# Optimization experiments

Hardware: AMD Instinct MI355X
Metric: run time of the kernel (lower is better)

The kernel has to match this reference:

```python
import jax, jax.numpy as jnp
import numpy as np

NUM_LEVELS = 16
BASE_RES = 16
T = 1 << 19            # hashmap size per level (log2_hashmap_size=19)
LEVEL_DIM = 2
SCALE = 2.0 ** (np.log2(2048.0 / 16.0) / (NUM_LEVELS - 1))  # desired_resolution=2048
PRIME1 = 2654435761
PRIME2 = 805459861
N_POINTS = 524288


def hash_encode(x, tables):
    # x: [N,3] in [0,1]; tables: [NUM_LEVELS, T, LEVEL_DIM]
    x = jnp.clip(x, 0.0, 1.0)
    feats = []
    for l in range(NUM_LEVELS):
        R = int(np.ceil(BASE_RES * SCALE ** l))
        pos = x * R                      # grid has R+1 vertices per axis
        p0f = jnp.floor(pos)
        w = pos - p0f                    # trilinear weights [N,3]
        p0 = p0f.astype(jnp.uint32)
        dense = (R + 1) ** 3 <= T
        acc = jnp.zeros((x.shape[0], LEVEL_DIM), dtype=tables.dtype)
        for c in range(8):               # 8 cube corners
            off = np.array([(c >> d) & 1 for d in range(3)], dtype=np.uint32)
            idx = jnp.minimum(p0 + off[None, :], jnp.uint32(R))
            if dense:
                flat = idx[:, 0] + jnp.uint32(R + 1) * idx[:, 1] + jnp.uint32((R + 1) ** 2) * idx[:, 2]
            else:
                flat = idx[:, 0] ^ (idx[:, 1] * jnp.uint32(PRIME1)) ^ (idx[:, 2] * jnp.uint32(PRIME2))
                flat = flat & jnp.uint32(T - 1)
            wc = jnp.prod(jnp.where(off[None, :] == 1, w, 1.0 - w), axis=-1)
            acc = acc + wc[:, None] * tables[l, flat]
        feats.append(acc)
    return jnp.concatenate(feats, axis=-1)  # [N, 32]


def pos_embed(x):
    # NeRF embedding: include input + sin/cos of 2^0..2^5 * x -> 3 + 36 = 39 dims
    outs = [x]
    for j in range(6):
        f = float(2 ** j)
        outs.append(jnp.sin(f * x))
        outs.append(jnp.cos(f * x))
    return jnp.concatenate(outs, axis=-1)


def wn_linear(h, v, g, b):
    # weight-norm: W = g * v / ||v||_row
    w = g[:, None] * v / jnp.linalg.norm(v, axis=1, keepdims=True)
    return h @ w.T + b


def softplus100(x):
    return jax.nn.softplus(100.0 * x) / 100.0


def setup_inputs() -> dict:
    key = jax.random.key(0)
    ks = jax.random.split(key, 8)
    x = jax.random.uniform(ks[0], (N_POINTS, 3), dtype=jnp.float32)
    tables = jax.random.uniform(ks[1], (NUM_LEVELS, T, LEVEL_DIM), minval=-1e-4, maxval=1e-4, dtype=jnp.float32)
    d_in_mlp = 3 + 36 + NUM_LEVELS * LEVEL_DIM  # 71
    dims = [d_in_mlp, 256, 256, 257]
    params = {}
    for l in range(3):
        fan_out = dims[l + 1]
        v = jax.random.normal(ks[2 + l], (dims[l + 1], dims[l]), dtype=jnp.float32) * np.sqrt(2.0 / fan_out)
        params[f'v{l}'] = v
        params[f'g{l}'] = jnp.linalg.norm(v, axis=1)  # weight_norm init: g = ||v||
        params[f'b{l}'] = jnp.zeros((dims[l + 1],), dtype=jnp.float32)
    return {'x': x, 'tables': tables, **params}


def reference(x, tables, v0, g0, b0, v1, g1, b1, v2, g2, b2):
    # object_center=0, object_scale=1, divide_factor=1 -> encoder sees x directly
    feat = hash_encode(x, tables)
    inp = jnp.concatenate([pos_embed(x), feat], axis=-1)  # [N, 71]
    h = softplus100(wn_linear(inp, v0, g0, b0))
    h = softplus100(wn_linear(h, v1, g1, b1))
    return wn_linear(h, v2, g2, b2)  # [N, 257] = sdf(1) + feature(256)
```

## Files before the change

### kernel.cpp

```cpp
#include <hip/hip_runtime.h>
#include <math.h>

typedef __bf16 bf16;
typedef __attribute__((ext_vector_type(8))) __bf16 bf16x8;
typedef __attribute__((ext_vector_type(4))) float f32x4;
typedef __attribute__((ext_vector_type(4))) short s16x4;

#define T_HASH (1u << 19)
#define PRIME1 2654435761u
#define PRIME2 805459861u

struct Levels { unsigned R[16]; unsigned mY[16]; unsigned mZ[16]; unsigned df[16]; };

__device__ __forceinline__ unsigned umin_(unsigned a, unsigned b) { return a < b ? a : b; }

__device__ __forceinline__ int swzoff(int row, int colByte) {
    return row * 512 + (colByte ^ ((row & 7) << 4));
}

__device__ __forceinline__ void stb(char* base, int row, int col, float v) {
    *(bf16*)(base + swzoff(row, col * 2)) = (bf16)v;
}
__device__ __forceinline__ void stw(char* base, int row, int col, unsigned short v) {
    *(unsigned short*)(base + swzoff(row, col * 2)) = v;
}

__device__ __forceinline__ float softplus100f(float v) {
    float u = v * 144.2695041f;
    float e = __builtin_amdgcn_exp2f(u);
    float y = __builtin_amdgcn_logf(1.f + e) * 0.006931471806f;
    return v > 0.25f ? v : y;
}

__device__ __forceinline__ unsigned short f2bfu(float v) {
    bf16 h = (bf16)v;
    return *(unsigned short*)&h;
}

__global__ void prep_weights(const float* __restrict__ v0, const float* __restrict__ g0,
                             const float* __restrict__ v1, const float* __restrict__ g1,
                             const float* __restrict__ v2, const float* __restrict__ g2,
                             unsigned short* __restrict__ W0, unsigned short* __restrict__ W1,
                             unsigned short* __restrict__ W2) {
    int r = blockIdx.x;
    int lane = threadIdx.x;
    const float* src = nullptr; const float* g = nullptr; unsigned short* dst; int K, Kp, row;
    if (r < 256)      { row = r;       src = v0 + row * 71;  g = g0; dst = W0 + row * 96;  K = 71;  Kp = 96;  }
    else if (r < 512) { row = r - 256; src = v1 + row * 256; g = g1; dst = W1 + row * 256; K = 256; Kp = 256; }
    else              { row = r - 512; if (row < 257) { src = v2 + row * 256; g = g2; }
                        dst = W2 + row * 256; K = 256; Kp = 256; }
    float ss = 0.f;
    if (src) for (int c = lane; c < K; c += 64) { float v = src[c]; ss += v * v; }
    for (int off = 32; off; off >>= 1) ss += __shfl_down(ss, off);
    ss = __shfl(ss, 0);
    float scale = src ? (g[row] / sqrtf(ss)) : 0.f;
    for (int c = lane; c < Kp; c += 64) {
        float v = (src && c < K) ? src[c] * scale : 0.f;
        dst[c] = f2bfu(v);
    }
}

__global__ void conv_tables(const float2* __restrict__ t, unsigned* __restrict__ tbf) {
    size_t i = (size_t)blockIdx.x * 256 + threadIdx.x;
    float2 e = t[i];
    tbf[i] = (unsigned)f2bfu(e.x) | ((unsigned)f2bfu(e.y) << 16);
}

__global__ __launch_bounds__(256, 8)
void encode_levels(const float* __restrict__ x, const unsigned* __restrict__ tbf,
                   unsigned* __restrict__ featsLM, Levels lv, int npts) {
    const int slot = blockIdx.x & 7, seq = blockIdx.x >> 3;
    const int l = slot + 8 * (seq & 1);
    const int group = seq >> 1;
    const unsigned Ru = lv.R[l], mY = lv.mY[l], mZ = lv.mZ[l];
    const bool dense = lv.df[l] != 0;
    const unsigned* __restrict__ tl = tbf + (size_t)l * T_HASH;
    unsigned* __restrict__ fout = featsLM + (size_t)l * npts;
    const float Rf = (float)Ru;
    const int base = group * 1024 + threadIdx.x;
#pragma unroll
    for (int k = 0; k < 4; ++k) {
        const int p = base + k * 256;
        float xr0 = x[p * 3 + 0], xr1 = x[p * 3 + 1], xr2 = x[p * 3 + 2];
        const float cx = fminf(fmaxf(xr0, 0.f), 1.f);
        const float cy = fminf(fmaxf(xr1, 0.f), 1.f);
        const float cz = fminf(fmaxf(xr2, 0.f), 1.f);
        float px = cx * Rf, py = cy * Rf, pz = cz * Rf;
        float fx = floorf(px), fy = floorf(py), fz = floorf(pz);
        float wx = px - fx, wy = py - fy, wz = pz - fz;
        unsigned ix = (unsigned)fx, iy = (unsigned)fy, iz = (unsigned)fz;
        unsigned xc0 = ix, xc1 = umin_(ix + 1u, Ru);
        unsigned y0 = iy * mY, y1 = umin_(iy + 1u, Ru) * mY;
        unsigned z0 = iz * mZ, z1 = umin_(iz + 1u, Ru) * mZ;
        unsigned yzA[4] = { y0 + z0, y1 + z0, y0 + z1, y1 + z1 };
        float w0x = 1.f - wx, w0y = 1.f - wy, w0z = 1.f - wz;
        float wyz[4] = { w0y * w0z, wy * w0z, w0y * wz, wy * wz };
        float a0 = 0.f, a1 = 0.f;
#pragma unroll
        for (int c = 0; c < 8; ++c) {
            const int ox = c & 1, cyz = c >> 1;
            unsigned xc = ox ? xc1 : xc0;
            unsigned gi = dense ? (xc + yzA[cyz])
                                : ((xc ^ yzA[cyz]) & (T_HASH - 1u));
            unsigned u = tl[gi];
            float ex = __uint_as_float(u << 16);
            float ey = __uint_as_float(u & 0xffff0000u);
            float wc = (ox ? wx : w0x) * wyz[cyz];
            a0 = fmaf(wc, ex, a0);
            a1 = fmaf(wc, ey, a1);
        }
        unsigned outw = (unsigned)f2bfu(a0) | ((unsigned)f2bfu(a1) << 16);
        __builtin_nontemporal_store(outw, &fout[p]);
    }
}


#define STG_STRIDE 260

template<int KSTEPS, int ROWLEN>
__device__ __forceinline__ void layer_mid(const char* __restrict__ inbuf,
                                          const unsigned short* __restrict__ W,
                                          const float* __restrict__ bias,
                                          char* __restrict__ outbuf, int tid) {
    const int lane = tid & 63, wave = tid >> 6;
    const int lrow = lane & 15, lk = lane >> 4;
    const unsigned short* __restrict__ wrow = W + (wave * 16 + lrow) * ROWLEN + lk * 8;
    f32x4 acc[4] = {};
    bf16x8 a_cur = *(const bf16x8*)(wrow);
#pragma unroll
    for (int ks = 0; ks < KSTEPS; ++ks) {
        const int k0 = ks * 32 + lk * 8;
        bf16x8 b[4];
#pragma unroll
        for (int pt = 0; pt < 4; ++pt)
            b[pt] = *(const bf16x8*)(inbuf + swzoff(pt * 16 + lrow, k0 * 2));
        bf16x8 a_next;
        if (ks + 1 < KSTEPS) a_next = *(const bf16x8*)(wrow + (ks + 1) * 32);
#pragma unroll
        for (int pt = 0; pt < 4; ++pt)
            acc[pt] = __builtin_amdgcn_mfma_f32_16x16x32_bf16(a_cur, b[pt], acc[pt], 0, 0, 0);
        a_cur = a_next;
    }
    const int c0 = wave * 16 + lk * 4;
    const float4 bv = *(const float4*)(bias + c0);
#pragma unroll
    for (int pt = 0; pt < 4; ++pt) {
        const int p = pt * 16 + lrow;
        s16x4 o;
        o.x = (short)f2bfu(softplus100f(acc[pt][0] + bv.x));
        o.y = (short)f2bfu(softplus100f(acc[pt][1] + bv.y));
        o.z = (short)f2bfu(softplus100f(acc[pt][2] + bv.z));
        o.w = (short)f2bfu(softplus100f(acc[pt][3] + bv.w));
        *(s16x4*)(outbuf + swzoff(p, c0 * 2)) = o;
    }
}

__device__ __forceinline__ void layer_fin(const char* __restrict__ inbuf,
                                          const unsigned short* __restrict__ W2,
                                          const float* __restrict__ b2,
                                          float* __restrict__ stg,
                                          float* __restrict__ out, int tid, int blk) {
    const int lane = tid & 63, wave = tid >> 6;
    const int lrow = lane & 15, lk = lane >> 4;
    const unsigned short* __restrict__ wrow = W2 + (wave * 16 + lrow) * 256 + lk * 8;
    f32x4 acc[4] = {};
    bf16x8 a_cur = *(const bf16x8*)(wrow);
#pragma unroll
    for (int ks = 0; ks < 8; ++ks) {
        const int k0 = ks * 32 + lk * 8;
        bf16x8 b[4];
#pragma unroll
        for (int pt = 0; pt < 4; ++pt)
            b[pt] = *(const bf16x8*)(inbuf + swzoff(pt * 16 + lrow, k0 * 2));
        bf16x8 a_next;
        if (ks < 7) a_next = *(const bf16x8*)(wrow + (ks + 1) * 32);
#pragma unroll
        for (int pt = 0; pt < 4; ++pt)
            acc[pt] = __builtin_amdgcn_mfma_f32_16x16x32_bf16(a_cur, b[pt], acc[pt], 0, 0, 0);
        a_cur = a_next;
    }
    const int p = tid >> 4, sub = tid & 15;
    float part = 0.f;
    {
        const unsigned short* __restrict__ w2r = W2 + 256 * 256 + sub * 16;
        bf16x8 h0 = *(const bf16x8*)(inbuf + swzoff(p, sub * 32));
        bf16x8 h1 = *(const bf16x8*)(inbuf + swzoff(p, sub * 32 + 16));
        bf16x8 w0 = *(const bf16x8*)(w2r);
        bf16x8 w1 = *(const bf16x8*)(w2r + 8);
#pragma unroll
        for (int j = 0; j < 8; ++j) {
            part = fmaf((float)h0[j], (float)w0[j], part);
            part = fmaf((float)h1[j], (float)w1[j], part);
        }
    }
#pragma unroll
    for (int m = 1; m < 16; m <<= 1) part += __shfl_xor(part, m);

    __syncthreads();
    const int c0 = wave * 16 + lk * 4;
    const float4 bv = *(const float4*)(b2 + c0);
#pragma unroll
    for (int pt = 0; pt < 4; ++pt) {
        const int pr = pt * 16 + lrow;
        f32x4 v;
        v[0] = acc[pt][0] + bv.x;
        v[1] = acc[pt][1] + bv.y;
        v[2] = acc[pt][2] + bv.z;
        v[3] = acc[pt][3] + bv.w;
        *(f32x4*)(stg + pr * STG_STRIDE + c0) = v;
    }
    if (sub == 0) stg[p * STG_STRIDE + 256] = part + b2[256];
    __syncthreads();
    float* __restrict__ dst = out + (size_t)blk * 16448;
#pragma unroll
    for (int r = 0; r < 4; ++r) {
        const int f0 = (r * 1024 + tid) * 4;
        const unsigned pp = ((unsigned)f0 * 65281u) >> 24;
        const int cc = f0 - (int)pp * 257;
        f32x4 v;
#pragma unroll
        for (int u = 0; u < 4; ++u) {
            int c2 = cc + u; unsigned p2 = pp;
            if (c2 >= 257) { c2 -= 257; p2++; }
            v[u] = stg[p2 * STG_STRIDE + c2];
        }
        *(f32x4*)(dst + f0) = v;
    }
    if (tid < 64) {
        const int f0 = 16384 + tid;
        const unsigned pp = ((unsigned)f0 * 65281u) >> 24;
        const int cc = f0 - (int)pp * 257;
        dst[f0] = stg[pp * STG_STRIDE + cc];
    }
}

__global__ __launch_bounds__(1024, 8)
void fused_net(const float* __restrict__ x, const float2* __restrict__ tables,
               const unsigned* __restrict__ featsLM,
               const unsigned short* __restrict__ W0, const unsigned short* __restrict__ W1,
               const unsigned short* __restrict__ W2,
               const float* __restrict__ b0, const float* __restrict__ b1, const float* __restrict__ b2,
               float* __restrict__ out, Levels lv, int npts) {
    __shared__ __align__(16) char smem[66560 + 256];
    unsigned* sR  = (unsigned*)(smem + 66560);
    unsigned* sMY = sR + 16;
    unsigned* sMZ = sR + 32;
    unsigned* sDF = sR + 48;
    char* buf0 = smem;
    char* buf1 = smem + 32768;
    float* stg = (float*)smem;
    const int tid = threadIdx.x;
    const int blk = blockIdx.x;

    if (tid >= 960) {
        int i = tid - 960;
        if (i < 16)      sR[i]  = lv.R[i];
        else if (i < 32) sMY[i - 16] = lv.mY[i - 16];
        else if (i < 48) sMZ[i - 32] = lv.mZ[i - 32];
        else             sDF[i - 48] = lv.df[i - 48];
    }
    __syncthreads();

    const int p = tid >> 4, sub = tid & 15;
    const float xr0 = x[(size_t)blk * 192 + p * 3 + 0];
    const float xr1 = x[(size_t)blk * 192 + p * 3 + 1];
    const float xr2 = x[(size_t)blk * 192 + p * 3 + 2];

    if (sub < 13) {
        int c0 = sub * 3;
#pragma unroll
        for (int u = 0; u < 3; ++u) {
            int c = c0 + u;
            if (c >= 39) break;
            float v;
            if (c < 3) v = (c == 0) ? xr0 : (c == 1 ? xr1 : xr2);
            else {
                int q = c - 3, j = q / 6, k = q - j * 6;
                int axis = (k < 3) ? k : k - 3;
                float xv = axis == 0 ? xr0 : (axis == 1 ? xr1 : xr2);
                float fx = (float)(1 << j) * xv;
                v = (k < 3) ? __sinf(fx) : __cosf(fx);
            }
            stb(buf0, p, c, v);
        }
    }
    for (int c = 71 + sub; c < 96; c += 16) stb(buf0, p, c, 0.f);

    if (featsLM) {
        const int l = sub;
        unsigned u = featsLM[(size_t)l * npts + blk * 64 + p];
        stw(buf0, p, 39 + 2 * l, (unsigned short)(u & 0xffffu));
        stw(buf0, p, 40 + 2 * l, (unsigned short)(u >> 16));
    } else {
        const int l = sub;
        const float cx = fminf(fmaxf(xr0, 0.f), 1.f);
        const float cy = fminf(fmaxf(xr1, 0.f), 1.f);
        const float cz = fminf(fmaxf(xr2, 0.f), 1.f);
        const unsigned Ru = sR[l], mY = sMY[l], mZ = sMZ[l];
        const bool dense = sDF[l] != 0;
        const unsigned lofs = (unsigned)l << 19;
        const float Rf = (float)Ru;
        float px = cx * Rf, py = cy * Rf, pz = cz * Rf;
        float fx = floorf(px), fy = floorf(py), fz = floorf(pz);
        float wx = px - fx, wy = py - fy, wz = pz - fz;
        unsigned ix = (unsigned)fx, iy = (unsigned)fy, iz = (unsigned)fz;
        unsigned xc0 = ix, xc1 = umin_(ix + 1u, Ru);
        unsigned y0 = iy * mY, y1 = umin_(iy + 1u, Ru) * mY;
        unsigned z0 = iz * mZ, z1 = umin_(iz + 1u, Ru) * mZ;
        unsigned yzA[4] = { y0 + z0 + lofs, y1 + z0 + lofs, y0 + z1 + lofs, y1 + z1 + lofs };
        unsigned yzX[4] = { y0 ^ z0, y1 ^ z0, y0 ^ z1, y1 ^ z1 };
        float w0x = 1.f - wx, w0y = 1.f - wy, w0z = 1.f - wz;
        float wyz[4] = { w0y * w0z, wy * w0z, w0y * wz, wy * wz };
        float a0 = 0.f, a1 = 0.f;
#pragma unroll
        for (int c = 0; c < 8; ++c) {
            const int ox = c & 1, cyz = c >> 1;
            unsigned xc = ox ? xc1 : xc0;
            unsigned fd = xc + yzA[cyz];
            unsigned fh = ((xc ^ yzX[cyz]) & (T_HASH - 1u)) + lofs;
            unsigned gi = dense ? fd : fh;
            float2 e2 = tables[gi];
            float wc = (ox ? wx : w0x) * wyz[cyz];
            a0 = fmaf(wc, e2.x, a0);
            a1 = fmaf(wc, e2.y, a1);
        }
        stb(buf0, p, 39 + 2 * l, a0);
        stb(buf0, p, 40 + 2 * l, a1);
    }
    __syncthreads();

    layer_mid<3, 96>(buf0, W0, b0, buf1, tid);
    __syncthreads();
    layer_mid<8, 256>(buf1, W1, b1, buf0, tid);
    __syncthreads();
    layer_fin(buf0, W2, b2, stg, out, tid, blk);
}

extern "C" void kernel_launch(void* const* d_in, const int* in_sizes, int n_in,
                              void* d_out, int out_size, void* d_ws, size_t ws_size,
                              hipStream_t stream) {
    const float*  x      = (const float*)d_in[0];
    const float2* tables = (const float2*)d_in[1];
    const float*  v0 = (const float*)d_in[2];
    const float*  g0 = (const float*)d_in[3];
    const float*  b0 = (const float*)d_in[4];
    const float*  v1 = (const float*)d_in[5];
    const float*  g1 = (const float*)d_in[6];
    const float*  b1 = (const float*)d_in[7];
    const float*  v2 = (const float*)d_in[8];
    const float*  g2 = (const float*)d_in[9];
    const float*  b2 = (const float*)d_in[10];

    unsigned short* W0 = (unsigned short*)d_ws;
    unsigned short* W1 = W0 + 256 * 96;
    unsigned short* W2 = W1 + 256 * 256;
    size_t ofs_tbf   = 319488;
    size_t ofs_feats = ofs_tbf + (size_t)16 * T_HASH * 4;
    size_t need      = ofs_feats + (size_t)16 * T_HASH * 4;
    unsigned* tbf     = (unsigned*)((char*)d_ws + ofs_tbf);
    unsigned* featsLM = (unsigned*)((char*)d_ws + ofs_feats);
    bool use_split = ws_size >= need;

    Levels lv;
    double SCALE = pow(2.0, log2(2048.0 / 16.0) / 15.0);
    for (int l = 0; l < 16; ++l) {
        double r = 16.0 * pow(SCALE, (double)l);
        unsigned R = (unsigned)ceil(r);
        lv.R[l] = R;
        unsigned long long s = (unsigned long long)R + 1;
        int dense = (s * s * s <= (unsigned long long)T_HASH) ? 1 : 0;
        lv.df[l] = dense;
        lv.mY[l] = dense ? (R + 1u) : PRIME1;
        lv.mZ[l] = dense ? (R + 1u) * (R + 1u) : PRIME2;
    }

    prep_weights<<<784, 64, 0, stream>>>(v0, g0, v1, g1, v2, g2, W0, W1, W2);

    int n = in_sizes[0] / 3;
    int nblk = n / 64;

    if (use_split) {
        conv_tables<<<16 * T_HASH / 256, 256, 0, stream>>>(tables, tbf);
        encode_levels<<<8 * (n / 1024) * 2, 256, 0, stream>>>(x, tbf, featsLM, lv, n);
        fused_net<<<nblk, 1024, 0, stream>>>(x, tables, featsLM, W0, W1, W2,
                                             b0, b1, b2, (float*)d_out, lv, n);
    } else {
        fused_net<<<nblk, 1024, 0, stream>>>(x, tables, nullptr, W0, W1, W2,
                                             b0, b1, b2, (float*)d_out, lv, n);
    }
}
```

Baseline: 626.9 us.

## Shrink fused MLP block to 32 points with 2x2 MFMA tiles per wave

```diff
diff --git a/kernel.cpp b/kernel.cpp
--- a/kernel.cpp
+++ b/kernel.cpp
@@ -124,34 +124,44 @@
                                           char* __restrict__ outbuf, int tid) {
     const int lane = tid & 63, wave = tid >> 6;
     const int lrow = lane & 15, lk = lane >> 4;
-    const unsigned short* __restrict__ wrow = W + (wave * 16 + lrow) * ROWLEN + lk * 8;
-    f32x4 acc[4] = {};
-    bf16x8 a_cur = *(const bf16x8*)(wrow);
+    const unsigned short* __restrict__ wr0 = W + (wave * 32 + lrow) * ROWLEN + lk * 8;
+    const unsigned short* __restrict__ wr1 = W + (wave * 32 + 16 + lrow) * ROWLEN + lk * 8;
+    f32x4 acc[2][2] = {};
+    bf16x8 a_cur[2] = { *(const bf16x8*)(wr0), *(const bf16x8*)(wr1) };
 #pragma unroll
     for (int ks = 0; ks < KSTEPS; ++ks) {
         const int k0 = ks * 32 + lk * 8;
-        bf16x8 b[4];
-#pragma unroll
-        for (int pt = 0; pt < 4; ++pt)
+        bf16x8 b[2];
+#pragma unroll
+        for (int pt = 0; pt < 2; ++pt)
             b[pt] = *(const bf16x8*)(inbuf + swzoff(pt * 16 + lrow, k0 * 2));
-        bf16x8 a_next;
-        if (ks + 1 < KSTEPS) a_next = *(const bf16x8*)(wrow + (ks + 1) * 32);
-#pragma unroll
-        for (int pt = 0; pt < 4; ++pt)
-            acc[pt] = __builtin_amdgcn_mfma_f32_16x16x32_bf16(a_cur, b[pt], acc[pt], 0, 0, 0);
-        a_cur = a_next;
-    }
-    const int c0 = wave * 16 + lk * 4;
-    const float4 bv = *(const float4*)(bias + c0);
-#pragma unroll
-    for (int pt = 0; pt < 4; ++pt) {
-        const int p = pt * 16 + lrow;
-        s16x4 o;
-        o.x = (short)f2bfu(softplus100f(acc[pt][0] + bv.x));
-        o.y = (short)f2bfu(softplus100f(acc[pt][1] + bv.y));
-        o.z = (short)f2bfu(softplus100f(acc[pt][2] + bv.z));
-        o.w = (short)f2bfu(softplus100f(acc[pt][3] + bv.w));
-        *(s16x4*)(outbuf + swzoff(p, c0 * 2)) = o;
+        bf16x8 a_next[2];
+        if (ks + 1 < KSTEPS) {
+            a_next[0] = *(const bf16x8*)(wr0 + (ks + 1) * 32);
+            a_next[1] = *(const bf16x8*)(wr1 + (ks + 1) * 32);
+        }
+#pragma unroll
+        for (int mr = 0; mr < 2; ++mr)
+#pragma unroll
+            for (int pt = 0; pt < 2; ++pt)
+                acc[mr][pt] = __builtin_amdgcn_mfma_f32_16x16x32_bf16(a_cur[mr], b[pt], acc[mr][pt], 0, 0, 0);
+        a_cur[0] = a_next[0];
+        a_cur[1] = a_next[1];
+    }
+#pragma unroll
+    for (int mr = 0; mr < 2; ++mr) {
+        const int c0 = wave * 32 + mr * 16 + lk * 4;
+        const float4 bv = *(const float4*)(bias + c0);
+#pragma unroll
+        for (int pt = 0; pt < 2; ++pt) {
+            const int p = pt * 16 + lrow;
+            s16x4 o;
+            o.x = (short)f2bfu(softplus100f(acc[mr][pt][0] + bv.x));
+            o.y = (short)f2bfu(softplus100f(acc[mr][pt][1] + bv.y));
+            o.z = (short)f2bfu(softplus100f(acc[mr][pt][2] + bv.z));
+            o.w = (short)f2bfu(softplus100f(acc[mr][pt][3] + bv.w));
+            *(s16x4*)(outbuf + swzoff(p, c0 * 2)) = o;
+        }
     }
 }
 
@@ -162,22 +172,29 @@
                                           float* __restrict__ out, int tid, int blk) {
     const int lane = tid & 63, wave = tid >> 6;
     const int lrow = lane & 15, lk = lane >> 4;
-    const unsigned short* __restrict__ wrow = W2 + (wave * 16 + lrow) * 256 + lk * 8;
-    f32x4 acc[4] = {};
-    bf16x8 a_cur = *(const bf16x8*)(wrow);
+    const unsigned short* __restrict__ wr0 = W2 + (wave * 32 + lrow) * 256 + lk * 8;
+    const unsigned short* __restrict__ wr1 = W2 + (wave * 32 + 16 + lrow) * 256 + lk * 8;
+    f32x4 acc[2][2] = {};
+    bf16x8 a_cur[2] = { *(const bf16x8*)(wr0), *(const bf16x8*)(wr1) };
 #pragma unroll
     for (int ks = 0; ks < 8; ++ks) {
         const int k0 = ks * 32 + lk * 8;
-        bf16x8 b[4];
-#pragma unroll
-        for (int pt = 0; pt < 4; ++pt)
+        bf16x8 b[2];
+#pragma unroll
+        for (int pt = 0; pt < 2; ++pt)
             b[pt] = *(const bf16x8*)(inbuf + swzoff(pt * 16 + lrow, k0 * 2));
-        bf16x8 a_next;
-        if (ks < 7) a_next = *(const bf16x8*)(wrow + (ks + 1) * 32);
-#pragma unroll
-        for (int pt = 0; pt < 4; ++pt)
-            acc[pt] = __builtin_amdgcn_mfma_f32_16x16x32_bf16(a_cur, b[pt], acc[pt], 0, 0, 0);
-        a_cur = a_next;
+        bf16x8 a_next[2];
+        if (ks < 7) {
+            a_next[0] = *(const bf16x8*)(wr0 + (ks + 1) * 32);
+            a_next[1] = *(const bf16x8*)(wr1 + (ks + 1) * 32);
+        }
+#pragma unroll
+        for (int mr = 0; mr < 2; ++mr)
+#pragma unroll
+            for (int pt = 0; pt < 2; ++pt)
+                acc[mr][pt] = __builtin_amdgcn_mfma_f32_16x16x32_bf16(a_cur[mr], b[pt], acc[mr][pt], 0, 0, 0);
+        a_cur[0] = a_next[0];
+        a_cur[1] = a_next[1];
     }
     const int p = tid >> 4, sub = tid & 15;
     float part = 0.f;
@@ -197,24 +214,27 @@
     for (int m = 1; m < 16; m <<= 1) part += __shfl_xor(part, m);
 
     __syncthreads();
-    const int c0 = wave * 16 + lk * 4;
-    const float4 bv = *(const float4*)(b2 + c0);
-#pragma unroll
-    for (int pt = 0; pt < 4; ++pt) {
-        const int pr = pt * 16 + lrow;
-        f32x4 v;
-        v[0] = acc[pt][0] + bv.x;
-        v[1] = acc[pt][1] + bv.y;
-        v[2] = acc[pt][2] + bv.z;
-        v[3] = acc[pt][3] + bv.w;
-        *(f32x4*)(stg + pr * STG_STRIDE + c0) = v;
+#pragma unroll
+    for (int mr = 0; mr < 2; ++mr) {
+        const int c0 = wave * 32 + mr * 16 + lk * 4;
+        const float4 bv = *(const float4*)(b2 + c0);
+#pragma unroll
+        for (int pt = 0; pt < 2; ++pt) {
+            const int pr = pt * 16 + lrow;
+            f32x4 v;
+            v[0] = acc[mr][pt][0] + bv.x;
+            v[1] = acc[mr][pt][1] + bv.y;
+            v[2] = acc[mr][pt][2] + bv.z;
+            v[3] = acc[mr][pt][3] + bv.w;
+            *(f32x4*)(stg + pr * STG_STRIDE + c0) = v;
+        }
     }
     if (sub == 0) stg[p * STG_STRIDE + 256] = part + b2[256];
     __syncthreads();
-    float* __restrict__ dst = out + (size_t)blk * 16448;
+    float* __restrict__ dst = out + (size_t)blk * 8224;
 #pragma unroll
     for (int r = 0; r < 4; ++r) {
-        const int f0 = (r * 1024 + tid) * 4;
+        const int f0 = (r * 512 + tid) * 4;
         const unsigned pp = ((unsigned)f0 * 65281u) >> 24;
         const int cc = f0 - (int)pp * 257;
         f32x4 v;
@@ -226,34 +246,34 @@
         }
         *(f32x4*)(dst + f0) = v;
     }
-    if (tid < 64) {
-        const int f0 = 16384 + tid;
+    if (tid < 32) {
+        const int f0 = 8192 + tid;
         const unsigned pp = ((unsigned)f0 * 65281u) >> 24;
         const int cc = f0 - (int)pp * 257;
         dst[f0] = stg[pp * STG_STRIDE + cc];
     }
 }
 
-__global__ __launch_bounds__(1024, 8)
+__global__ __launch_bounds__(512, 8)
 void fused_net(const float* __restrict__ x, const float2* __restrict__ tables,
                const unsigned* __restrict__ featsLM,
                const unsigned short* __restrict__ W0, const unsigned short* __restrict__ W1,
                const unsigned short* __restrict__ W2,
                const float* __restrict__ b0, const float* __restrict__ b1, const float* __restrict__ b2,
                float* __restrict__ out, Levels lv, int npts) {
-    __shared__ __align__(16) char smem[66560 + 256];
-    unsigned* sR  = (unsigned*)(smem + 66560);
+    __shared__ __align__(16) char smem[33280 + 256];
+    unsigned* sR  = (unsigned*)(smem + 33280);
     unsigned* sMY = sR + 16;
     unsigned* sMZ = sR + 32;
     unsigned* sDF = sR + 48;
     char* buf0 = smem;
-    char* buf1 = smem + 32768;
+    char* buf1 = smem + 16384;
     float* stg = (float*)smem;
     const int tid = threadIdx.x;
     const int blk = blockIdx.x;
 
-    if (tid >= 960) {
-        int i = tid - 960;
+    if (tid >= 448) {
+        int i = tid - 448;
         if (i < 16)      sR[i]  = lv.R[i];
         else if (i < 32) sMY[i - 16] = lv.mY[i - 16];
         else if (i < 48) sMZ[i - 32] = lv.mZ[i - 32];
@@ -262,9 +282,9 @@
     __syncthreads();
 
     const int p = tid >> 4, sub = tid & 15;
-    const float xr0 = x[(size_t)blk * 192 + p * 3 + 0];
-    const float xr1 = x[(size_t)blk * 192 + p * 3 + 1];
-    const float xr2 = x[(size_t)blk * 192 + p * 3 + 2];
+    const float xr0 = x[(size_t)blk * 96 + p * 3 + 0];
+    const float xr1 = x[(size_t)blk * 96 + p * 3 + 1];
+    const float xr2 = x[(size_t)blk * 96 + p * 3 + 2];
 
     if (sub < 13) {
         int c0 = sub * 3;
@@ -288,7 +308,7 @@
 
     if (featsLM) {
         const int l = sub;
-        unsigned u = featsLM[(size_t)l * npts + blk * 64 + p];
+        unsigned u = featsLM[(size_t)l * npts + blk * 32 + p];
         stw(buf0, p, 39 + 2 * l, (unsigned short)(u & 0xffffu));
         stw(buf0, p, 40 + 2 * l, (unsigned short)(u >> 16));
     } else {
@@ -377,15 +397,15 @@
     prep_weights<<<784, 64, 0, stream>>>(v0, g0, v1, g1, v2, g2, W0, W1, W2);
 
     int n = in_sizes[0] / 3;
-    int nblk = n / 64;
+    int nblk = n / 32;
 
     if (use_split) {
         conv_tables<<<16 * T_HASH / 256, 256, 0, stream>>>(tables, tbf);
         encode_levels<<<8 * (n / 1024) * 2, 256, 0, stream>>>(x, tbf, featsLM, lv, n);
-        fused_net<<<nblk, 1024, 0, stream>>>(x, tables, featsLM, W0, W1, W2,
-                                             b0, b1, b2, (float*)d_out, lv, n);
+        fused_net<<<nblk, 512, 0, stream>>>(x, tables, featsLM, W0, W1, W2,
+                                            b0, b1, b2, (float*)d_out, lv, n);
     } else {
-        fused_net<<<nblk, 1024, 0, stream>>>(x, tables, nullptr, W0, W1, W2,
-                                             b0, b1, b2, (float*)d_out, lv, n);
-    }
-}
+        fused_net<<<nblk, 512, 0, stream>>>(x, tables, nullptr, W0, W1, W2,
+                                            b0, b1, b2, (float*)d_out, lv, n);
+    }
+}
```

New measurement: 835.8 us. +33.3%, slower.
